# Performance work log

Measured on AMD Instinct MI355X. Metric: run time of the kernel, lower is better.

The kernel has to match this reference:

```python
import jax, jax.numpy as jnp
import numpy as np

B, BATCH, N, M, L1, NITER = 8, 4096, 16, 128, 16, 5


def setup_inputs() -> dict:
    key = jax.random.key(0)
    k1, k2, k3 = jax.random.split(key, 3)
    h = jax.random.normal(k1, (B, BATCH, N, M), dtype=jnp.float32)
    wd_init = jax.random.normal(k2, (B, BATCH, L1, N), dtype=jnp.float32)
    hyp = jax.random.uniform(k3, (NITER, B + 1), dtype=jnp.float32) * 0.01  # step sizes
    return {"h": h, "wd_init": wd_init, "hyp": hyp, "n": N, "l1": L1, "b": B, "num_of_iter": NITER}


def _herm(x):
    # inputs are real float32, so conj() in the original is the identity
    return jnp.swapaxes(x, -1, -2)


def reference(h, wd_init, hyp, n, l1, b, num_of_iter):
    batch, m = h.shape[1], h.shape[3]
    eye = jnp.eye(n, dtype=h.dtype)
    nb = jnp.asarray(n * b, h.dtype)

    def renorm_scale(prod):
        # prod: (b, batch, r, c); torch: sqrt(n*b / sum_b ||prod||_F^2) -> (batch,)
        fro2 = jnp.sum(prod * prod, axis=(-2, -1))  # (b, batch)
        return jnp.sqrt(nb / jnp.sum(fro2, axis=0))[:, None, None]  # (batch,1,1)

    def cov(h_, wa_, wd_):
        t = h_ @ wa_ @ wd_  # (..., n, n)
        return eye + t @ _herm(t)

    def grad_wa(wa_, wd_):
        inv_t = _herm(jnp.linalg.inv(cov(h, wa_, wd_)))  # (b,batch,n,n)
        f2 = jnp.sum(_herm(h) @ inv_t @ h @ wa_ @ wd_ @ _herm(wd_), axis=0) / b  # (batch,m,l1)
        return jnp.broadcast_to(f2[None], (b, batch, m, l1))

    def grad_wd_i(h_i, wa0, wd_i):
        inv_t = _herm(jnp.linalg.inv(cov(h_i, wa0, wd_i)))  # (batch,n,n)
        return _herm(wa0) @ _herm(h_i) @ inv_t @ h_i @ wa0 @ wd_i / b  # (batch,l1,n)

    # init: wa from svd of mean channel (numpy svd in original -> constant wrt grads)
    _, _, vh = jnp.linalg.svd(jnp.mean(h, axis=0), full_matrices=True)  # (batch,m,m)
    vh = jax.lax.stop_gradient(vh)
    wa = jnp.broadcast_to(vh[:, :, :l1][None], (b, batch, m, l1))
    wd = renorm_scale(wa @ wd_init) * wd_init  # (b,batch,l1,n)

    objs = []
    for x in range(num_of_iter):
        wa_t = wa + hyp[x, 0] * grad_wa(wa, wd)
        wa = renorm_scale(wa_t @ wd) * wa_t
        wd_t = wd
        for i in range(b):  # sequential inner projected-gradient updates (as in original)
            g = grad_wd_i(h[i], wa[0], wd[i])
            wd_t = wd_t.at[i].set(wd[i] + hyp[x, i + 1] * g)
            wd = renorm_scale(wa @ wd_t) * wd_t
        _, logdet = jnp.linalg.slogdet(cov(h, wa, wd))  # det > 0 (I + PSD)
        objs.append(jnp.sum(logdet, axis=0) / b)  # (batch,)
    obj = jnp.stack(objs, axis=0)  # (num_of_iter, batch)
    return obj.T, wa, wd
```

## Files before the change

### kernel.cpp

```cpp
#include <hip/hip_runtime.h>
#include <math.h>

#define NBATCH 4096


__device__ __forceinline__ float wave64_sum(float v){
  #pragma unroll
  for(int off=32; off; off>>=1) v += __shfl_xor(v, off, 64);
  return v;
}

__device__ __forceinline__ void slartgf(float f, float g, float* cs, float* sn, float* r){
  if (g == 0.0f){ *cs = 1.0f; *sn = 0.0f; *r = f; }
  else if (f == 0.0f){ *cs = 0.0f; *sn = copysignf(1.0f, g); *r = fabsf(g); }
  else {
    float d = sqrtf(f*f + g*g);
    *cs = fabsf(f)/d;
    float rr = copysignf(d, f);
    *r = rr;
    *sn = g/rr;
  }
}

__device__ __forceinline__ void slas2f(float f, float g, float hh, float* ssmin, float* ssmax){
  float fa=fabsf(f), ga=fabsf(g), ha=fabsf(hh);
  float fhmn=fminf(fa,ha), fhmx=fmaxf(fa,ha);
  if (fhmn == 0.0f){
    *ssmin = 0.0f;
    if (fhmx == 0.0f) *ssmax = ga;
    else { float mx=fmaxf(fhmx,ga), mn=fminf(fhmx,ga); float q=mn/mx; *ssmax = mx*sqrtf(1.0f+q*q); }
  } else {
    if (ga < fhmx){
      float as_=1.0f+fhmn/fhmx;
      float at_=(fhmx-fhmn)/fhmx;
      float au_=(ga/fhmx); au_=au_*au_;
      float c_=2.0f/(sqrtf(as_*as_+au_)+sqrtf(at_*at_+au_));
      *ssmin=fhmn*c_;
      *ssmax=fhmx/c_;
    } else {
      float au_=fhmx/ga;
      if (au_==0.0f){ *ssmin=(fhmn*fhmx)/ga; *ssmax=ga; }
      else {
        float as_=1.0f+fhmn/fhmx;
        float at_=(fhmx-fhmn)/fhmx;
        float t1=as_*au_, t2=at_*au_;
        float c_=1.0f/(sqrtf(1.0f+t1*t1)+sqrtf(1.0f+t2*t2));
        float sm=(fhmn*c_)*au_;
        *ssmin=sm+sm;
        *ssmax=ga/(c_+c_);
      }
    }
  }
}

__device__ __forceinline__ void slasv2f(float f, float g, float hh,
    float* ssmin, float* ssmax, float* snr, float* csr, float* snl, float* csl){
  const float EPS2 = 5.9604644775390625e-08f;
  float ft=f, fa=fabsf(f), ht=hh, ha=fabsf(hh);
  int pmax=1;
  bool swap_=(ha>fa);
  if (swap_){ pmax=3; float tmp=ft; ft=ht; ht=tmp; tmp=fa; fa=ha; ha=tmp; }
  float gt=g, ga=fabsf(g);
  float clt=0.f, crt=0.f, slt=0.f, srt=0.f;
  if (ga==0.0f){ *ssmin=ha; *ssmax=fa; clt=1.f; crt=1.f; slt=0.f; srt=0.f; }
  else {
    bool gasmal=true;
    if (ga>fa){
      pmax=2;
      if ((fa/ga) < EPS2){
        gasmal=false;
        *ssmax=ga;
        if (ha>1.0f) *ssmin=fa/(ga/ha); else *ssmin=(fa/ga)*ha;
        clt=1.f; slt=ht/gt; srt=1.f; crt=ft/gt;
      }
    }
    if (gasmal){
      float d_=fa-ha;
      float l_;
      if (d_==fa) l_=1.0f; else l_=d_/fa;
      float m_=gt/ft;
      float t_=2.0f-l_;
      float mm=m_*m_, tt=t_*t_;
      float s_=sqrtf(tt+mm);
      float r_;
      if (l_==0.0f) r_=fabsf(m_); else r_=sqrtf(l_*l_+mm);
      float a_=0.5f*(s_+r_);
      *ssmin=ha/a_;
      *ssmax=fa*a_;
      if (mm==0.0f){
        if (l_==0.0f) t_=copysignf(2.0f,ft)*copysignf(1.0f,gt);
        else t_=gt/copysignf(d_,ft)+m_/t_;
      } else {
        t_=(m_/(s_+t_)+m_/(r_+l_))*(1.0f+a_);
      }
      l_=sqrtf(t_*t_+4.0f);
      crt=2.0f/l_;
      srt=t_/l_;
      clt=(crt+srt*m_)/a_;
      slt=(ht/ft)*srt/a_;
    }
  }
  if (swap_){ *csl=srt; *snl=crt; *csr=slt; *snr=clt; }
  else { *csl=clt; *snl=slt; *csr=crt; *snr=srt; }
  float tsign=0.f;
  if (pmax==1) tsign=copysignf(1.f,*csr)*copysignf(1.f,*csl)*copysignf(1.f,f);
  if (pmax==2) tsign=copysignf(1.f,*snr)*copysignf(1.f,*csl)*copysignf(1.f,g);
  if (pmax==3) tsign=copysignf(1.f,*snr)*copysignf(1.f,*snl)*copysignf(1.f,hh);
  *ssmax=copysignf(*ssmax,tsign);
  *ssmin=copysignf(*ssmin,tsign*copysignf(1.f,f)*copysignf(1.f,hh));
}

__global__ __launch_bounds__(64) void init_kernel(
    const float* __restrict__ h,
    const float* __restrict__ wd_init,
    float* __restrict__ out_wa,
    float* __restrict__ out_wd)
{
  const int batch = blockIdx.x;
  const int lane  = threadIdx.x;
  if (batch >= NBATCH) return;

  __shared__ float A[16][128];
  __shared__ float Qc[128][16];
  __shared__ float Lm[16][16];
  __shared__ float VTs[16][16];
  __shared__ float Wtop[16][16];
  __shared__ float tauL[16], tq[16], tp[16];
  __shared__ float dB[16], eB[16];
  volatile __shared__ float dsh[17];
  volatile __shared__ float esh[17];

  for(int e0=lane; e0<2048; e0+=64){
    int nn=e0>>7, mmi=e0&127;
    float s=0.f;
    #pragma unroll
    for(int i=0;i<8;i++) s += h[((size_t)(i*NBATCH+batch))*2048 + nn*128 + mmi];
    A[nn][mmi]=s*0.125f;
  }
  __syncthreads();

  for(int i=0;i<16;i++){
    float part=0.f;
    for(int j=i+1+lane;j<128;j+=64){ float v=A[i][j]; part+=v*v; }
    float xn2=wave64_sum(part);
    float alpha=A[i][i];
    float tau,beta,scal;
    if (xn2==0.0f){ tau=0.f; beta=alpha; scal=0.f; }
    else {
      beta=-copysignf(sqrtf(alpha*alpha+xn2), alpha);
      tau=(beta-alpha)/beta;
      scal=1.0f/(alpha-beta);
    }
    if (tau!=0.0f){
      for(int j=i+1+lane;j<128;j+=64) A[i][j]*=scal;
    }
    if (lane==0){ A[i][i]=beta; tauL[i]=tau; }
    __syncthreads();
    if (tau!=0.0f){
      for(int r=i+1;r<16;r++){
        float p=0.f;
        for(int j=i+1+lane;j<128;j+=64) p += A[r][j]*A[i][j];
        float w=wave64_sum(p) + A[r][i];
        float tw=tau*w;
        for(int j=i+1+lane;j<128;j+=64) A[r][j]-=tw*A[i][j];
        if (lane==0) A[r][i]-=tw;
      }
    }
    __syncthreads();
  }

  for(int j=0;j<16;j++){
    float c0 = (lane==j)?1.0f:0.0f;
    float c1 = 0.0f;
    for(int i=0;i<16;i++){
      float tau=tauL[i];
      float p=0.f;
      if (lane>i) p += A[i][lane]*c0;
      else if (lane==i) p += c0;
      p += A[i][64+lane]*c1;
      float w=wave64_sum(p);
      if (tau!=0.0f){
        float tw=tau*w;
        if (lane==i) c0 -= tw;
        else if (lane>i) c0 -= tw*A[i][lane];
        c1 -= tw*A[i][64+lane];
      }
    }
    Qc[lane][j]=c0;
    Qc[64+lane][j]=c1;
  }
  __syncthreads();

  for(int e0=lane;e0<256;e0+=64){ int r=e0>>4,c=e0&15; Lm[r][c]=(c<=r)?A[r][c]:0.0f; }
  __syncthreads();

  for(int i=0;i<16;i++){
    float alpha=Lm[i][i];
    float xn2=0.f;
    for(int r=i+1;r<16;r++){ float v=Lm[r][i]; xn2+=v*v; }
    float tauqi,beta,scal;
    if (xn2==0.0f){ tauqi=0.f; beta=alpha; scal=0.f; }
    else { beta=-copysignf(sqrtf(alpha*alpha+xn2),alpha); tauqi=(beta-alpha)/beta; scal=1.0f/(alpha-beta); }
    __syncthreads();
    if (lane==0){
      tq[i]=tauqi; dB[i]=beta;
      if (tauqi!=0.0f) for(int r=i+1;r<16;r++) Lm[r][i]*=scal;
    }
    __syncthreads();
    if (tauqi!=0.0f && lane>i && lane<16){
      int c=lane;
      float w=Lm[i][c];
      for(int r=i+1;r<16;r++) w += Lm[r][i]*Lm[r][c];
      float tw=tauqi*w;
      Lm[i][c]-=tw;
      for(int r=i+1;r<16;r++) Lm[r][c]-=tw*Lm[r][i];
    }
    __syncthreads();
    if (i<15){
      float alph2=Lm[i][i+1];
      float yn2=0.f;
      for(int c=i+2;c<16;c++){ float v=Lm[i][c]; yn2+=v*v; }
      float taupi,beta2,scal2;
      if (yn2==0.0f){ taupi=0.f; beta2=alph2; scal2=0.f; }
      else { beta2=-copysignf(sqrtf(alph2*alph2+yn2),alph2); taupi=(beta2-alph2)/beta2; scal2=1.0f/(alph2-beta2); }
      __syncthreads();
      if (lane==0){
        tp[i]=taupi; eB[i]=beta2;
        if (taupi!=0.0f) for(int c=i+2;c<16;c++) Lm[i][c]*=scal2;
      }
      __syncthreads();
      if (taupi!=0.0f && lane>i && lane<16){
        int r=lane;
        float w=Lm[r][i+1];
        for(int c=i+2;c<16;c++) w += Lm[i][c]*Lm[r][c];
        float tw=taupi*w;
        Lm[r][i+1]-=tw;
        for(int c=i+2;c<16;c++) Lm[r][c]-=tw*Lm[i][c];
      }
      __syncthreads();
    } else {
      if (lane==0) tp[i]=0.0f;
      __syncthreads();
    }
  }

  if (lane==0){
    for(int k=1;k<=16;k++) dsh[k]=dB[k-1];
    for(int k=1;k<=15;k++) esh[k]=eB[k-1];
  }
  if (lane<16){
    for(int r=0;r<16;r++) VTs[r][lane]=(r==lane)?1.0f:0.0f;
  }
  __syncthreads();
  {
    const float EPSB = 5.9604644775390625e-08f;
    const float UNFL = 1.1754943508222875e-38f;
    const float tolb = 10.0f*EPSB;
    float sminoa;
    {
      sminoa=fabsf(dsh[1]);
      if (sminoa!=0.0f){
        float mu=sminoa;
        for(int k=2;k<=16;k++){
          mu=fabsf(dsh[k])*(mu/(mu+fabsf(esh[k-1])));
          sminoa=fminf(sminoa,mu);
          if (sminoa==0.0f) break;
        }
      }
      sminoa*=0.25f;
    }
    float thresh=fmaxf(tolb*sminoa, 6.0f*256.0f*UNFL);
    int maxitdivn=6*16, iterdivn=0, iter_=-1;
    int oldll=-1, oldm=-1, idir=0;
    int mq=16;
    float sminl=0.0f;
    int guard=0;
    while (guard++ < 4000){
      if (mq<=1) break;
      if (iter_>=16){ iter_-=16; iterdivn++; if (iterdivn>=maxitdivn) break; }
      float smax=fabsf(dsh[mq]);
      int ll=0; bool split=false;
      for(int lll=1;lll<=mq-1;lll++){
        int l2=mq-lll;
        float abss=fabsf(dsh[l2]);
        float abse=fabsf(esh[l2]);
        if (abse<=thresh){ ll=l2; split=true; break; }
        smax=fmaxf(smax,fmaxf(abss,abse));
      }
      if (split){
        if (lane==0) esh[ll]=0.0f;
        if (ll==mq-1){ mq=mq-1; continue; }
        ll=ll+1;
      } else ll=1;
      if (ll==mq-1){
        float sigmn,sigmx,sinr,cosr,sinl_,cosl_;
        slasv2f(dsh[mq-1],esh[mq-1],dsh[mq],&sigmn,&sigmx,&sinr,&cosr,&sinl_,&cosl_);
        if (lane==0){ dsh[mq-1]=sigmx; esh[mq-1]=0.0f; dsh[mq]=sigmn; }
        if (lane<16){
          float x0=VTs[mq-2][lane], y0=VTs[mq-1][lane];
          VTs[mq-2][lane]=cosr*x0+sinr*y0;
          VTs[mq-1][lane]=cosr*y0-sinr*x0;
        }
        mq-=2;
        continue;
      }
      if (ll>oldm || mq<oldll)
        idir=(fabsf(dsh[ll])>=fabsf(dsh[mq]))?1:2;
      bool conv=false;
      if (idir==1){
        if (fabsf(esh[mq-1])<=tolb*fabsf(dsh[mq])){ if(lane==0) esh[mq-1]=0.0f; conv=true; }
        if (!conv){
          float mu=fabsf(dsh[ll]); sminl=mu;
          for(int lll=ll;lll<=mq-1;lll++){
            if (fabsf(esh[lll])<=tolb*mu){ if(lane==0) esh[lll]=0.0f; conv=true; break; }
            mu=fabsf(dsh[lll+1])*(mu/(mu+fabsf(esh[lll])));
            sminl=fminf(sminl,mu);
          }
        }
      } else {
        if (fabsf(esh[ll])<=tolb*fabsf(dsh[ll])){ if(lane==0) esh[ll]=0.0f; conv=true; }
        if (!conv){
          float mu=fabsf(dsh[mq]); sminl=mu;
          for(int lll=mq-1;lll>=ll;lll--){
            if (fabsf(esh[lll])<=tolb*mu){ if(lane==0) esh[lll]=0.0f; conv=true; break; }
            mu=fabsf(dsh[lll])*(mu/(mu+fabsf(esh[lll])));
            sminl=fminf(sminl,mu);
          }
        }
      }
      if (conv) continue;
      oldll=ll; oldm=mq;
      float shift=0.0f, rdum;
      if (!( 16.0f*tolb*(sminl/smax) <= fmaxf(EPSB, 0.01f*tolb) )){
        float sll;
        if (idir==1){ sll=fabsf(dsh[ll]); slas2f(dsh[mq-1],esh[mq-1],dsh[mq],&shift,&rdum); }
        else        { sll=fabsf(dsh[mq]); slas2f(dsh[ll],esh[ll],dsh[ll+1],&shift,&rdum); }
        if (sll>0.0f){ float q=shift/sll; if (q*q<EPSB) shift=0.0f; }
      }
      iter_ += mq-ll;
      if (shift==0.0f){
        if (idir==1){
          float cs=1.0f, oldcs=1.0f, sn=0.0f, oldsn=0.0f, r1, r2;
          for(int i=ll;i<=mq-1;i++){
            slartgf(dsh[i]*cs, esh[i], &cs, &sn, &r1);
            if (i>ll){ if(lane==0) esh[i-1]=oldsn*r1; }
            slartgf(oldcs*r1, dsh[i+1]*sn, &oldcs, &oldsn, &r2);
            if (lane==0) dsh[i]=r2;
            if (lane<16){
              float lo=VTs[i-1][lane], hi=VTs[i][lane];
              VTs[i][lane]  =cs*hi-sn*lo;
              VTs[i-1][lane]=sn*hi+cs*lo;
            }
          }
          float hval=dsh[mq]*cs;
          float nd=hval*oldcs, ne=hval*oldsn;
          if (lane==0){ dsh[mq]=nd; esh[mq-1]=(fabsf(ne)<=thresh)?0.0f:ne; }
        } else {
          float cs=1.0f, oldcs=1.0f, sn=0.0f, oldsn=0.0f, r1, r2;
          for(int i=mq;i>=ll+1;i--){
            slartgf(dsh[i]*cs, esh[i-1], &cs, &sn, &r1);
            if (i<mq){ if(lane==0) esh[i]=oldsn*r1; }
            slartgf(oldcs*r1, dsh[i-1]*sn, &oldcs, &oldsn, &r2);
            if (lane==0) dsh[i]=r2;
            if (lane<16){
              float lo=VTs[i-2][lane], hi=VTs[i-1][lane];
              float c_=oldcs, s_=-oldsn;
              VTs[i-1][lane]=c_*hi-s_*lo;
              VTs[i-2][lane]=s_*hi+c_*lo;
            }
          }
          float hval=dsh[ll]*cs;
          float nd=hval*oldcs, ne=hval*oldsn;
          if (lane==0){ dsh[ll]=nd; esh[ll]=(fabsf(ne)<=thresh)?0.0f:ne; }
        }
      } else {
        if (idir==1){
          float dll=dsh[ll];
          float f=(fabsf(dll)-shift)*(copysignf(1.0f,dll)+shift/dll);
          float g=esh[ll];
          float cosr,sinr,cosl_,sinl_,r1;
          for(int i=ll;i<=mq-1;i++){
            slartgf(f,g,&cosr,&sinr,&r1);
            if (i>ll){ if(lane==0) esh[i-1]=r1; }
            float di=dsh[i], ei=esh[i], dip=dsh[i+1];
            f=cosr*di+sinr*ei;
            float ei1=cosr*ei-sinr*di;
            g=sinr*dip;
            float dip1=cosr*dip;
            slartgf(f,g,&cosl_,&sinl_,&r1);
            if (lane==0) dsh[i]=r1;
            f=cosl_*ei1+sinl_*dip1;
            float dip2=cosl_*dip1-sinl_*ei1;
            float eip2=0.0f;
            if (i<mq-1){
              float eip=esh[i+1];
              g=sinl_*eip;
              eip2=cosl_*eip;
            }
            if (lane==0){
              esh[i]=ei1;
              dsh[i+1]=dip2;
              if (i<mq-1) esh[i+1]=eip2;
            }
            if (lane<16){
              float lo=VTs[i-1][lane], hi=VTs[i][lane];
              VTs[i][lane]  =cosr*hi-sinr*lo;
              VTs[i-1][lane]=sinr*hi+cosr*lo;
            }
          }
          if (lane==0) esh[mq-1]=(fabsf(f)<=thresh)?0.0f:f;
        } else {
          float dm=dsh[mq];
          float f=(fabsf(dm)-shift)*(copysignf(1.0f,dm)+shift/dm);
          float g=esh[mq-1];
          float cosr,sinr,cosl_,sinl_,r1;
          for(int i=mq;i>=ll+1;i--){
            slartgf(f,g,&cosr,&sinr,&r1);
            if (i<mq){ if(lane==0) esh[i]=r1; }
            float di=dsh[i], eim=esh[i-1], dim=dsh[i-1];
            f=cosr*di+sinr*eim;
            float eim1=cosr*eim-sinr*di;
            g=sinr*dim;
            float dim1=cosr*dim;
            slartgf(f,g,&cosl_,&sinl_,&r1);
            if (lane==0) dsh[i]=r1;
            f=cosl_*eim1+sinl_*dim1;
            float dim2=cosl_*dim1-sinl_*eim1;
            float eim3=0.0f;
            if (i>ll+1){
              float e2=esh[i-2];
              g=sinl_*e2;
              eim3=cosl_*e2;
            }
            if (lane==0){
              esh[i-1]=eim1;
              dsh[i-1]=dim2;
              if (i>ll+1) esh[i-2]=eim3;
            }
            if (lane<16){
              float lo=VTs[i-2][lane], hi=VTs[i-1][lane];
              float c_=cosl_, s_=-sinl_;
              VTs[i-1][lane]=c_*hi-s_*lo;
              VTs[i-2][lane]=s_*hi+c_*lo;
            }
          }
          if (lane==0) esh[ll]=(fabsf(f)<=thresh)?0.0f:f;
        }
      }
    }
    for(int k=1;k<=16;k++){
      float dv=dsh[k];
      if (dv<0.0f){
        if (lane==0) dsh[k]=-dv;
        if (lane<16) VTs[k-1][lane]=-VTs[k-1][lane];
      }
    }
    for(int i=1;i<=15;i++){
      int isub=1; float smn=dsh[1];
      for(int j=2;j<=17-i;j++){ float dj=dsh[j]; if (dj<=smn){ isub=j; smn=dj; } }
      if (isub!=17-i){
        if (lane==0){ dsh[isub]=dsh[17-i]; dsh[17-i]=smn; }
        if (lane<16){ float tv=VTs[isub-1][lane]; VTs[isub-1][lane]=VTs[16-i][lane]; VTs[16-i][lane]=tv; }
      }
    }
  }
  __syncthreads();

  for(int i=14;i>=0;i--){
    float tau=tp[i];
    if (tau!=0.0f && lane<16){
      int r=lane;
      float w=VTs[r][i+1];
      for(int c=i+2;c<16;c++) w += VTs[r][c]*Lm[i][c];
      float tw=tau*w;
      VTs[r][i+1]-=tw;
      for(int c=i+2;c<16;c++) VTs[r][c]-=tw*Lm[i][c];
    }
  }
  __syncthreads();

  for(int e0=lane;e0<256;e0+=64){
    int r=e0>>4, j=e0&15;
    float s=0.f;
    #pragma unroll
    for(int c=0;c<16;c++) s += VTs[r][c]*Qc[c][j];
    Wtop[r][j]=s;
  }
  __syncthreads();
  for(int e0=lane;e0<2048;e0+=64){
    int r=e0>>4, j=e0&15;
    out_wa[(size_t)batch*2048 + e0] = (r<16)?Wtop[r][j]:Qc[r][j];
  }

  float part=0.f;
  for(int i=0;i<8;i++){
    const float* wdi = wd_init + ((size_t)(i*NBATCH+batch))*256;
    for(int e=lane;e<256;e+=64) ((float*)Lm)[e]=wdi[e];
    __syncthreads();
    for(int e0=lane;e0<2048;e0+=64){
      int r=e0>>4, j=e0&15;
      float s=0.f;
      #pragma unroll
      for(int c=0;c<16;c++){
        float wav=(r<16)?Wtop[r][c]:Qc[r][c];
        s += wav*((float*)Lm)[c*16+j];
      }
      part += s*s;
    }
    __syncthreads();
  }
  float fro2=wave64_sum(part);
  float scal2=sqrtf(128.0f/fro2);
  for(int i=0;i<8;i++){
    const float* wdi = wd_init + ((size_t)(i*NBATCH+batch))*256;
    float* wdo = out_wd + ((size_t)(i*NBATCH+batch))*256;
    for(int e=lane;e<256;e+=64) wdo[e]=scal2*wdi[e];
  }
}

__global__ __launch_bounds__(256) void iter_kernel(
    const float* __restrict__ h,
    const float* __restrict__ hyp,
    float* __restrict__ out_obj,
    float* __restrict__ out_wa,
    float* __restrict__ out_wd)
{
  const int batch = blockIdx.x;
  const int t = threadIdx.x;
  if (batch >= NBATCH) return;

  __shared__ float Wf[2048];
  __shared__ __align__(16) float Hs[2048];
  __shared__ float Uf[2048];
  __shared__ float Wdf[2048];
  __shared__ float Wdtf[2048];
  __shared__ float Cvf[2048];
  __shared__ float F2f[2048];
  __shared__ float Gmf[256];
  __shared__ float T1f[256];
  __shared__ float T2f[256];
  __shared__ float T3f[256];
  __shared__ float redbuf[4];
  __shared__ float bcv[2];
  __shared__ float hyps[45];
  __shared__ float logdets[8];

  const int r16 = t>>4, c16 = t&15;

  {
    const float* src = out_wa + (size_t)batch*2048;
    for(int e=t;e<2048;e+=256) Wf[e]=src[e];
    for(int i=0;i<8;i++){
      const float* s2 = out_wd + ((size_t)(i*NBATCH+batch))*256;
      Wdf[i*256+t]=s2[t];
    }
    if (t<45) hyps[t]=hyp[t];
  }
  __syncthreads();

  auto stage_h = [&](int i){
    const float4* h4 = reinterpret_cast<const float4*>(h + ((size_t)(i*NBATCH+batch))*2048);
    float4* s4 = reinterpret_cast<float4*>(Hs);
    s4[t]=h4[t];
    s4[t+256]=h4[t+256];
  };
  auto compute_u = [&](int i){
    const float4* Hs4 = reinterpret_cast<const float4*>(Hs);
    float s=0.f;
    #pragma unroll
    for(int m4=0;m4<32;m4++){
      float4 hv=Hs4[r16*32+m4];
      s += hv.x*Wf[(m4*4+0)*16+c16];
      s += hv.y*Wf[(m4*4+1)*16+c16];
      s += hv.z*Wf[(m4*4+2)*16+c16];
      s += hv.w*Wf[(m4*4+3)*16+c16];
    }
    Uf[i*256+t]=s;
  };
  auto block_red = [&](float v)->float{
    #pragma unroll
    for(int off=32;off;off>>=1) v += __shfl_xor(v, off, 64);
    if ((t&63)==0) redbuf[t>>6]=v;
    __syncthreads();
    if (t==0) bcv[0]=redbuf[0]+redbuf[1]+redbuf[2]+redbuf[3];
    __syncthreads();
    return bcv[0];
  };
  auto batched_gj = [&](){
    int ii=t>>5, ss=t&31;
    float logacc=0.f;
    for(int k=0;k<16;k++){
      float piv=Cvf[ii*256+k*16+k];
      float rk8[8],ck8[8],cur8[8];
      #pragma unroll
      for(int q=0;q<8;q++){
        int e=ss*8+q; int rr=e>>4, cc=e&15;
        rk8[q]=Cvf[ii*256+k*16+cc];
        ck8[q]=Cvf[ii*256+rr*16+k];
        cur8[q]=Cvf[ii*256+e];
      }
      __syncthreads();
      float pinv=1.0f/piv;
      if (ss==0) logacc += logf(piv);
      #pragma unroll
      for(int q=0;q<8;q++){
        int e=ss*8+q; int rr=e>>4, cc=e&15;
        float v;
        if (rr==k) v=(cc==k)?pinv:rk8[q]*pinv;
        else if (cc==k) v=-ck8[q]*pinv;
        else v=cur8[q]-ck8[q]*pinv*rk8[q];
        Cvf[ii*256+e]=v;
      }
      __syncthreads();
    }
    if (ss==0) logdets[ii]=logacc;
    __syncthreads();
  };
  auto build_cov_all = [&](){
    for(int i=0;i<8;i++){
      float s=0.f;
      #pragma unroll
      for(int k=0;k<16;k++) s += Uf[i*256+r16*16+k]*Wdf[i*256+k*16+c16];
      T1f[t]=s;
      __syncthreads();
      float cv=(r16==c16)?1.0f:0.0f;
      #pragma unroll
      for(int k=0;k<16;k++) cv += T1f[r16*16+k]*T1f[c16*16+k];
      Cvf[i*256+t]=cv;
      __syncthreads();
    }
  };

  for(int i=0;i<8;i++){ stage_h(i); __syncthreads(); compute_u(i); __syncthreads(); }

  for(int x=0;x<5;x++){
    build_cov_all();
    batched_gj();
    if (x>0 && t==0){
      float s=0.f;
      for(int i=0;i<8;i++) s+=logdets[i];
      out_obj[batch*5+(x-1)]=s*0.125f;
    }
    for(int e=t;e<2048;e+=256) F2f[e]=0.f;
    __syncthreads();
    for(int i=0;i<8;i++){
      float s=0.f;
      #pragma unroll
      for(int k=0;k<16;k++) s += Cvf[i*256+k*16+r16]*Uf[i*256+k*16+c16];
      T1f[t]=s; __syncthreads();
      s=0.f;
      #pragma unroll
      for(int k=0;k<16;k++) s += T1f[r16*16+k]*Wdf[i*256+k*16+c16];
      T2f[t]=s; __syncthreads();
      s=0.f;
      #pragma unroll
      for(int k=0;k<16;k++) s += T2f[r16*16+k]*Wdf[i*256+c16*16+k];
      T3f[t]=s; __syncthreads();
      stage_h(i); __syncthreads();
      {
        int mm=t>>1, l0=(t&1)*8;
        float a0=0,a1=0,a2=0,a3=0,a4=0,a5=0,a6=0,a7=0;
        #pragma unroll
        for(int nn=0;nn<16;nn++){
          float hv=Hs[nn*128+mm];
          const float* T3r=&T3f[nn*16+l0];
          a0+=hv*T3r[0]; a1+=hv*T3r[1]; a2+=hv*T3r[2]; a3+=hv*T3r[3];
          a4+=hv*T3r[4]; a5+=hv*T3r[5]; a6+=hv*T3r[6]; a7+=hv*T3r[7];
        }
        float* F2r=&F2f[mm*16+l0];
        F2r[0]+=a0; F2r[1]+=a1; F2r[2]+=a2; F2r[3]+=a3;
        F2r[4]+=a4; F2r[5]+=a5; F2r[6]+=a6; F2r[7]+=a7;
      }
      __syncthreads();
    }
    {
      float hyp0=hyps[x*9]*0.125f;
      for(int e=t;e<2048;e+=256) Wf[e] += hyp0*F2f[e];
      __syncthreads();
      float s=0.f;
      #pragma unroll 8
      for(int mmi=0;mmi<128;mmi++) s += Wf[mmi*16+r16]*Wf[mmi*16+c16];
      Gmf[t]=s;
      __syncthreads();
      float part=0.f;
      for(int j=0;j<8;j++){
        float gw=0.f;
        #pragma unroll
        for(int k=0;k<16;k++) gw += Gmf[r16*16+k]*Wdf[j*256+k*16+c16];
        part += gw*Wdf[j*256+t];
      }
      float fro2=block_red(part);
      float scal=sqrtf(128.0f/fro2);
      for(int e=t;e<2048;e+=256) Wf[e]*=scal;
      Gmf[t]*=scal*scal;
      __syncthreads();
    }
    for(int i=0;i<8;i++){ stage_h(i); __syncthreads(); compute_u(i); __syncthreads(); }
    for(int e=t;e<2048;e+=256) Wdtf[e]=Wdf[e];
    __syncthreads();
    for(int i=0;i<8;i++){
      float s=0.f;
      #pragma unroll
      for(int k=0;k<16;k++) s += Uf[i*256+r16*16+k]*Wdf[i*256+k*16+c16];
      T1f[t]=s; __syncthreads();
      float cv=(r16==c16)?1.0f:0.0f;
      #pragma unroll
      for(int k=0;k<16;k++) cv += T1f[r16*16+k]*T1f[c16*16+k];
      T2f[t]=cv; __syncthreads();
      for(int k=0;k<16;k++){
        float piv=T2f[k*16+k];
        float rk=T2f[k*16+c16];
        float ck=T2f[r16*16+k];
        float cur=T2f[t];
        __syncthreads();
        float pinv=1.0f/piv;
        float v;
        if (r16==k) v=(c16==k)?pinv:rk*pinv;
        else if (c16==k) v=-ck*pinv;
        else v=cur-ck*pinv*rk;
        T2f[t]=v;
        __syncthreads();
      }
      s=0.f;
      #pragma unroll
      for(int k=0;k<16;k++) s += Uf[i*256+k*16+r16]*T2f[c16*16+k];
      T1f[t]=s; __syncthreads();
      s=0.f;
      #pragma unroll
      for(int k=0;k<16;k++) s += T1f[r16*16+k]*Uf[i*256+k*16+c16];
      T3f[t]=s; __syncthreads();
      {
        float g=0.f;
        #pragma unroll
        for(int k=0;k<16;k++) g += T3f[r16*16+k]*Wdf[i*256+k*16+c16];
        g*=0.125f;
        Wdtf[i*256+t]=Wdf[i*256+t]+hyps[x*9+i+1]*g;
      }
      __syncthreads();
      {
        float part=0.f;
        for(int j=0;j<8;j++){
          float gw=0.f;
          #pragma unroll
          for(int k=0;k<16;k++) gw += Gmf[r16*16+k]*Wdtf[j*256+k*16+c16];
          part += gw*Wdtf[j*256+t];
        }
        float fro2=block_red(part);
        float scal=sqrtf(128.0f/fro2);
        for(int e=t;e<2048;e+=256) Wdf[e]=scal*Wdtf[e];
      }
      __syncthreads();
    }
  }
  build_cov_all();
  batched_gj();
  if (t==0){
    float s=0.f;
    for(int i=0;i<8;i++) s+=logdets[i];
    out_obj[batch*5+4]=s*0.125f;
  }
  __syncthreads();
  for(int i=0;i<8;i++){
    float* dst = out_wa + ((size_t)(i*NBATCH+batch))*2048;
    for(int e=t;e<2048;e+=256) dst[e]=Wf[e];
  }
  for(int i=0;i<8;i++){
    float* dst = out_wd + ((size_t)(i*NBATCH+batch))*256;
    dst[t]=Wdf[i*256+t];
  }
}

extern "C" void kernel_launch(void* const* d_in, const int* in_sizes, int n_in,
                              void* d_out, int out_size, void* d_ws, size_t ws_size,
                              hipStream_t stream)
{
  (void)in_sizes; (void)n_in; (void)d_ws; (void)ws_size; (void)out_size;
  const float* h   = (const float*)d_in[0];
  const float* wdi = (const float*)d_in[1];
  const float* hyp = (const float*)d_in[2];
  float* out = (float*)d_out;
  float* out_obj = out;
  float* out_wa  = out + (size_t)NBATCH*5;
  float* out_wd  = out_wa + (size_t)8*NBATCH*128*16;

  init_kernel<<<NBATCH, 64, 0, stream>>>(h, wdi, out_wa, out_wd);
  iter_kernel<<<NBATCH, 256, 0, stream>>>(h, hyp, out_obj, out_wa, out_wd);
}
```

Baseline: 6.291 ms.

## Restructure iteration kernel into per-wave 16x16 chains with swizzled shared memory

Rewrites the iteration kernel so each wave processes its own channels' 16x16 covariance, Gauss-Jordan inversion and gradient chain, using compiler barriers in place of block-wide syncs. Shared memory shrinks: fewer buffers, half-size H staging, and an XOR-style rotate swizzle to avoid bank conflicts. The renormalisation is folded lazily into the next step, and launch bounds request higher occupancy. The init kernel keeps Q columns in registers and adds syncs in the SVD loop. The main risks are wave-level races that rely on implicit lockstep, and serialisation of the inner updates onto one wave.

```diff
diff --git a/kernel.cpp b/kernel.cpp
--- a/kernel.cpp
+++ b/kernel.cpp
@@ -3,12 +3,16 @@
 
 #define NBATCH 4096
 
+#define WBAR() asm volatile("" ::: "memory")
+
+__device__ __forceinline__ int SW(int r, int c){ return (r<<4) | (((c)+(r))&15); }
 
 __device__ __forceinline__ float wave64_sum(float v){
   #pragma unroll
   for(int off=32; off; off>>=1) v += __shfl_xor(v, off, 64);
   return v;
 }
+
 
 __device__ __forceinline__ void slartgf(float f, float g, float* cs, float* sn, float* r){
   if (g == 0.0f){ *cs = 1.0f; *sn = 0.0f; *r = f; }
@@ -118,17 +122,16 @@
 {
   const int batch = blockIdx.x;
   const int lane  = threadIdx.x;
-  if (batch >= NBATCH) return;
 
   __shared__ float A[16][128];
-  __shared__ float Qc[128][16];
   __shared__ float Lm[16][16];
   __shared__ float VTs[16][16];
   __shared__ float Wtop[16][16];
-  __shared__ float tauL[16], tq[16], tp[16];
+  __shared__ float Qtop[256];
+  __shared__ float tauL[16], tp[16];
   __shared__ float dB[16], eB[16];
-  volatile __shared__ float dsh[17];
-  volatile __shared__ float esh[17];
+  __shared__ float dsh[17];
+  __shared__ float esh[17];
 
   for(int e0=lane; e0<2048; e0+=64){
     int nn=e0>>7, mmi=e0&127;
@@ -169,6 +172,8 @@
     __syncthreads();
   }
 
+  float qc0[16], qc1[16];
+  #pragma unroll
   for(int j=0;j<16;j++){
     float c0 = (lane==j)?1.0f:0.0f;
     float c1 = 0.0f;
@@ -186,8 +191,12 @@
         c1 -= tw*A[i][64+lane];
       }
     }
-    Qc[lane][j]=c0;
-    Qc[64+lane][j]=c1;
+    qc0[j]=c0;
+    qc1[j]=c1;
+  }
+  if (lane<16){
+    #pragma unroll
+    for(int j=0;j<16;j++) Qtop[lane*16+j]=qc0[j];
   }
   __syncthreads();
 
@@ -203,7 +212,7 @@
     else { beta=-copysignf(sqrtf(alpha*alpha+xn2),alpha); tauqi=(beta-alpha)/beta; scal=1.0f/(alpha-beta); }
     __syncthreads();
     if (lane==0){
-      tq[i]=tauqi; dB[i]=beta;
+      dB[i]=beta;
       if (tauqi!=0.0f) for(int r=i+1;r<16;r++) Lm[r][i]*=scal;
     }
     __syncthreads();
@@ -289,18 +298,21 @@
       }
       if (split){
         if (lane==0) esh[ll]=0.0f;
+        __syncthreads();
         if (ll==mq-1){ mq=mq-1; continue; }
         ll=ll+1;
       } else ll=1;
       if (ll==mq-1){
         float sigmn,sigmx,sinr,cosr,sinl_,cosl_;
         slasv2f(dsh[mq-1],esh[mq-1],dsh[mq],&sigmn,&sigmx,&sinr,&cosr,&sinl_,&cosl_);
+        __syncthreads();
         if (lane==0){ dsh[mq-1]=sigmx; esh[mq-1]=0.0f; dsh[mq]=sigmn; }
         if (lane<16){
           float x0=VTs[mq-2][lane], y0=VTs[mq-1][lane];
           VTs[mq-2][lane]=cosr*x0+sinr*y0;
           VTs[mq-1][lane]=cosr*y0-sinr*x0;
         }
+        __syncthreads();
         mq-=2;
         continue;
       }
@@ -328,7 +340,7 @@
           }
         }
       }
-      if (conv) continue;
+      if (conv){ __syncthreads(); continue; }
       oldll=ll; oldm=mq;
       float shift=0.0f, rdum;
       if (!( 16.0f*tolb*(sminl/smax) <= fmaxf(EPSB, 0.01f*tolb) )){
@@ -351,10 +363,12 @@
               VTs[i][lane]  =cs*hi-sn*lo;
               VTs[i-1][lane]=sn*hi+cs*lo;
             }
+            __syncthreads();
           }
           float hval=dsh[mq]*cs;
           float nd=hval*oldcs, ne=hval*oldsn;
           if (lane==0){ dsh[mq]=nd; esh[mq-1]=(fabsf(ne)<=thresh)?0.0f:ne; }
+          __syncthreads();
         } else {
           float cs=1.0f, oldcs=1.0f, sn=0.0f, oldsn=0.0f, r1, r2;
           for(int i=mq;i>=ll+1;i--){
@@ -368,10 +382,12 @@
               VTs[i-1][lane]=c_*hi-s_*lo;
               VTs[i-2][lane]=s_*hi+c_*lo;
             }
+            __syncthreads();
           }
           float hval=dsh[ll]*cs;
           float nd=hval*oldcs, ne=hval*oldsn;
           if (lane==0){ dsh[ll]=nd; esh[ll]=(fabsf(ne)<=thresh)?0.0f:ne; }
+          __syncthreads();
         }
       } else {
         if (idir==1){
@@ -407,8 +423,10 @@
               VTs[i][lane]  =cosr*hi-sinr*lo;
               VTs[i-1][lane]=sinr*hi+cosr*lo;
             }
+            __syncthreads();
           }
           if (lane==0) esh[mq-1]=(fabsf(f)<=thresh)?0.0f:f;
+          __syncthreads();
         } else {
           float dm=dsh[mq];
           float f=(fabsf(dm)-shift)*(copysignf(1.0f,dm)+shift/dm);
@@ -443,8 +461,10 @@
               VTs[i-1][lane]=c_*hi-s_*lo;
               VTs[i-2][lane]=s_*hi+c_*lo;
             }
+            __syncthreads();
           }
           if (lane==0) esh[ll]=(fabsf(f)<=thresh)?0.0f:f;
+          __syncthreads();
         }
       }
     }
@@ -454,6 +474,7 @@
         if (lane==0) dsh[k]=-dv;
         if (lane<16) VTs[k-1][lane]=-VTs[k-1][lane];
       }
+      __syncthreads();
     }
     for(int i=1;i<=15;i++){
       int isub=1; float smn=dsh[1];
@@ -462,6 +483,7 @@
         if (lane==0){ dsh[isub]=dsh[17-i]; dsh[17-i]=smn; }
         if (lane<16){ float tv=VTs[isub-1][lane]; VTs[isub-1][lane]=VTs[16-i][lane]; VTs[16-i][lane]=tv; }
       }
+      __syncthreads();
     }
   }
   __syncthreads();
@@ -476,38 +498,44 @@
       VTs[r][i+1]-=tw;
       for(int c=i+2;c<16;c++) VTs[r][c]-=tw*Lm[i][c];
     }
-  }
-  __syncthreads();
+    __syncthreads();
+  }
 
   for(int e0=lane;e0<256;e0+=64){
     int r=e0>>4, j=e0&15;
     float s=0.f;
     #pragma unroll
-    for(int c=0;c<16;c++) s += VTs[r][c]*Qc[c][j];
+    for(int c=0;c<16;c++) s += VTs[r][c]*Qtop[c*16+j];
     Wtop[r][j]=s;
   }
   __syncthreads();
-  for(int e0=lane;e0<2048;e0+=64){
-    int r=e0>>4, j=e0&15;
-    out_wa[(size_t)batch*2048 + e0] = (r<16)?Wtop[r][j]:Qc[r][j];
-  }
-
+
+  {
+    float* wab = out_wa + (size_t)batch*2048;
+    #pragma unroll
+    for(int j=0;j<16;j++){
+      wab[lane*16+j]      = (lane<16)? Wtop[lane][j] : qc0[j];
+      wab[(lane+64)*16+j] = qc1[j];
+    }
+  }
+
+  float wrow[16];
+  #pragma unroll
+  for(int c=0;c<16;c++) wrow[c] = (lane<16)? Wtop[lane][c] : qc0[c];
+  float* wdL = (float*)Lm;
   float part=0.f;
   for(int i=0;i<8;i++){
     const float* wdi = wd_init + ((size_t)(i*NBATCH+batch))*256;
-    for(int e=lane;e<256;e+=64) ((float*)Lm)[e]=wdi[e];
-    __syncthreads();
-    for(int e0=lane;e0<2048;e0+=64){
-      int r=e0>>4, j=e0&15;
-      float s=0.f;
-      #pragma unroll
-      for(int c=0;c<16;c++){
-        float wav=(r<16)?Wtop[r][c]:Qc[r][c];
-        s += wav*((float*)Lm)[c*16+j];
-      }
-      part += s*s;
-    }
-    __syncthreads();
+    __syncthreads();
+    for(int e=lane;e<256;e+=64) wdL[e]=wdi[e];
+    __syncthreads();
+    #pragma unroll
+    for(int j=0;j<16;j++){
+      float s0=0.f, s1=0.f;
+      #pragma unroll
+      for(int c=0;c<16;c++){ float wv=wdL[c*16+j]; s0 += wrow[c]*wv; s1 += qc1[c]*wv; }
+      part += s0*s0 + s1*s1;
+    }
   }
   float fro2=wave64_sum(part);
   float scal2=sqrtf(128.0f/fro2);
@@ -518,7 +546,7 @@
   }
 }
 
-__global__ __launch_bounds__(256) void iter_kernel(
+__global__ __launch_bounds__(256,4) void iter_kernel(
     const float* __restrict__ h,
     const float* __restrict__ hyp,
     float* __restrict__ out_obj,
@@ -527,246 +555,341 @@
 {
   const int batch = blockIdx.x;
   const int t = threadIdx.x;
-  if (batch >= NBATCH) return;
+  const int wave = t>>6, lane = t&63;
+  const int r16 = t>>4, c16 = t&15;
+  const int ls = lane>>4, cc = lane&15;
 
   __shared__ float Wf[2048];
-  __shared__ __align__(16) float Hs[2048];
   __shared__ float Uf[2048];
-  __shared__ float Wdf[2048];
-  __shared__ float Wdtf[2048];
-  __shared__ float Cvf[2048];
-  __shared__ float F2f[2048];
-  __shared__ float Gmf[256];
-  __shared__ float T1f[256];
-  __shared__ float T2f[256];
-  __shared__ float T3f[256];
-  __shared__ float redbuf[4];
-  __shared__ float bcv[2];
-  __shared__ float hyps[45];
-  __shared__ float logdets[8];
-
-  const int r16 = t>>4, c16 = t&15;
+  __shared__ float Kf[2048];
+  __shared__ float Wd[2048];
+  __shared__ __align__(16) float Hs[1024];
+  __shared__ float Gm[256];
+  __shared__ float misc[24];
+
+  auto chain_K = [&](int ch, bool wlog){
+    float* U = Uf + ch*256;
+    float* W = Wd + ch*256;
+    float* A = Kf + ch*256;
+    float* B = Hs + wave*256;
+    #pragma unroll
+    for(int q=0;q<4;q++){
+      int rr=q*4+ls; float s=0.f;
+      #pragma unroll
+      for(int k=0;k<16;k++) s += U[rr*16+k]*W[SW(k,cc)];
+      A[SW(rr,cc)]=s;
+    }
+    WBAR();
+    #pragma unroll
+    for(int q=0;q<4;q++){
+      int rr=q*4+ls; float s=(rr==cc)?1.0f:0.0f;
+      #pragma unroll
+      for(int k=0;k<16;k++) s += A[SW(rr,k)]*A[SW(cc,k)];
+      B[SW(rr,cc)]=s;
+    }
+    WBAR();
+    float logacc=0.f;
+    for(int k=0;k<16;k++){
+      float piv=B[SW(k,k)];
+      float pinv=1.0f/piv;
+      if (wlog) logacc += logf(piv);
+      float rkv=B[SW(k,cc)];
+      float ck[4],cu[4];
+      #pragma unroll
+      for(int q=0;q<4;q++){ int rr=q*4+ls; ck[q]=B[SW(rr,k)]; cu[q]=B[SW(rr,cc)]; }
+      WBAR();
+      #pragma unroll
+      for(int q=0;q<4;q++){
+        int rr=q*4+ls; float v;
+        if (rr==k) v=(cc==k)?pinv:rkv*pinv;
+        else if (cc==k) v=-ck[q]*pinv;
+        else v=cu[q]-ck[q]*pinv*rkv;
+        B[SW(rr,cc)]=v;
+      }
+      WBAR();
+    }
+    if (wlog && lane==0) misc[ch]=logacc;
+    #pragma unroll
+    for(int q=0;q<4;q++){
+      int rr=q*4+ls; float s=0.f;
+      #pragma unroll
+      for(int k=0;k<16;k++) s += B[SW(k,rr)]*U[k*16+cc];
+      A[SW(rr,cc)]=s;
+    }
+    WBAR();
+    #pragma unroll
+    for(int q=0;q<4;q++){
+      int rr=q*4+ls; float s=0.f;
+      #pragma unroll
+      for(int k=0;k<16;k++) s += A[SW(rr,k)]*W[SW(k,cc)];
+      B[SW(rr,cc)]=s;
+    }
+    WBAR();
+    #pragma unroll
+    for(int q=0;q<4;q++){
+      int rr=q*4+ls; float s=0.f;
+      #pragma unroll
+      for(int k=0;k<16;k++) s += B[SW(rr,k)]*W[SW(cc,k)];
+      A[SW(rr,cc)]=s;
+    }
+    WBAR();
+  };
+
+  auto inner_step = [&](int i, int x, bool first){
+    float sc;
+    if (first) sc = 1.0f;
+    else {
+      float fs=0.f;
+      #pragma unroll
+      for(int j=0;j<8;j++) fs += misc[8+j];
+      sc = sqrtf(128.0f/fs);
+    }
+    float* U = Uf + i*256;
+    float* W = Wd + i*256;
+    float* A = Hs;
+    float* B = Hs + 256;
+    #pragma unroll
+    for(int q=0;q<4;q++){
+      int rr=q*4+ls; float s=0.f;
+      #pragma unroll
+      for(int k=0;k<16;k++) s += U[rr*16+k]*(sc*W[SW(k,cc)]);
+      A[SW(rr,cc)]=s;
+    }
+    WBAR();
+    #pragma unroll
+    for(int q=0;q<4;q++){
+      int rr=q*4+ls; float s=(rr==cc)?1.0f:0.0f;
+      #pragma unroll
+      for(int k=0;k<16;k++) s += A[SW(rr,k)]*A[SW(cc,k)];
+      B[SW(rr,cc)]=s;
+    }
+    WBAR();
+    for(int k=0;k<16;k++){
+      float piv=B[SW(k,k)];
+      float pinv=1.0f/piv;
+      float rkv=B[SW(k,cc)];
+      float ck[4],cu[4];
+      #pragma unroll
+      for(int q=0;q<4;q++){ int rr=q*4+ls; ck[q]=B[SW(rr,k)]; cu[q]=B[SW(rr,cc)]; }
+      WBAR();
+      #pragma unroll
+      for(int q=0;q<4;q++){
+        int rr=q*4+ls; float v;
+        if (rr==k) v=(cc==k)?pinv:rkv*pinv;
+        else if (cc==k) v=-ck[q]*pinv;
+        else v=cu[q]-ck[q]*pinv*rkv;
+        B[SW(rr,cc)]=v;
+      }
+      WBAR();
+    }
+    #pragma unroll
+    for(int q=0;q<4;q++){
+      int rr=q*4+ls; float s=0.f;
+      #pragma unroll
+      for(int k=0;k<16;k++) s += U[k*16+rr]*B[SW(cc,k)];
+      A[SW(rr,cc)]=s;
+    }
+    WBAR();
+    #pragma unroll
+    for(int q=0;q<4;q++){
+      int rr=q*4+ls; float s=0.f;
+      #pragma unroll
+      for(int k=0;k<16;k++) s += A[SW(rr,k)]*U[k*16+cc];
+      B[SW(rr,cc)]=s;
+    }
+    WBAR();
+    float hypi = hyp[x*9+i+1];
+    float wnew[4];
+    #pragma unroll
+    for(int q=0;q<4;q++){
+      int rr=q*4+ls; float g=0.f;
+      #pragma unroll
+      for(int k=0;k<16;k++) g += B[SW(rr,k)]*(sc*W[SW(k,cc)]);
+      g*=0.125f;
+      wnew[q] = sc*W[SW(rr,cc)] + hypi*g;
+    }
+    WBAR();
+    #pragma unroll
+    for(int q=0;q<4;q++){ int rr=q*4+ls; W[SW(rr,cc)]=wnew[q]; }
+    WBAR();
+    float part=0.f;
+    #pragma unroll
+    for(int q=0;q<4;q++){
+      int rr=q*4+ls; float gw=0.f;
+      #pragma unroll
+      for(int k=0;k<16;k++) gw += Gm[rr*16+k]*W[SW(k,cc)];
+      part += gw*W[SW(rr,cc)];
+    }
+    part = wave64_sum(part);
+    if (lane==0) misc[8+i]=part;
+  };
+
+  auto stage_and_u = [&](int ch, int half){
+    const float4* h4 = (const float4*)(h + ((size_t)(ch*NBATCH+batch))*2048);
+    __syncthreads();
+    ((float4*)Hs)[t] = h4[half*256+t];
+    __syncthreads();
+    if ((r16>>3)==half){
+      const float4* H4=(const float4*)Hs;
+      float s=0.f;
+      #pragma unroll
+      for(int m4=0;m4<32;m4++){
+        float4 hv=H4[(r16&7)*32+m4];
+        s += hv.x*Wf[(m4*4+0)*16+c16];
+        s += hv.y*Wf[(m4*4+1)*16+c16];
+        s += hv.z*Wf[(m4*4+2)*16+c16];
+        s += hv.w*Wf[(m4*4+3)*16+c16];
+      }
+      Uf[ch*256+r16*16+c16]=s;
+    }
+  };
 
   {
     const float* src = out_wa + (size_t)batch*2048;
     for(int e=t;e<2048;e+=256) Wf[e]=src[e];
-    for(int i=0;i<8;i++){
-      const float* s2 = out_wd + ((size_t)(i*NBATCH+batch))*256;
-      Wdf[i*256+t]=s2[t];
-    }
-    if (t<45) hyps[t]=hyp[t];
+    for(int ch=0;ch<8;ch++){
+      const float* s2 = out_wd + ((size_t)(ch*NBATCH+batch))*256;
+      Wd[ch*256+SW(r16,c16)] = s2[t];
+    }
+    if (t<8) misc[8+t]=16.0f;
   }
   __syncthreads();
-
-  auto stage_h = [&](int i){
-    const float4* h4 = reinterpret_cast<const float4*>(h + ((size_t)(i*NBATCH+batch))*2048);
-    float4* s4 = reinterpret_cast<float4*>(Hs);
-    s4[t]=h4[t];
-    s4[t+256]=h4[t+256];
-  };
-  auto compute_u = [&](int i){
-    const float4* Hs4 = reinterpret_cast<const float4*>(Hs);
-    float s=0.f;
-    #pragma unroll
-    for(int m4=0;m4<32;m4++){
-      float4 hv=Hs4[r16*32+m4];
-      s += hv.x*Wf[(m4*4+0)*16+c16];
-      s += hv.y*Wf[(m4*4+1)*16+c16];
-      s += hv.z*Wf[(m4*4+2)*16+c16];
-      s += hv.w*Wf[(m4*4+3)*16+c16];
-    }
-    Uf[i*256+t]=s;
-  };
-  auto block_red = [&](float v)->float{
-    #pragma unroll
-    for(int off=32;off;off>>=1) v += __shfl_xor(v, off, 64);
-    if ((t&63)==0) redbuf[t>>6]=v;
-    __syncthreads();
-    if (t==0) bcv[0]=redbuf[0]+redbuf[1]+redbuf[2]+redbuf[3];
-    __syncthreads();
-    return bcv[0];
-  };
-  auto batched_gj = [&](){
-    int ii=t>>5, ss=t&31;
-    float logacc=0.f;
-    for(int k=0;k<16;k++){
-      float piv=Cvf[ii*256+k*16+k];
-      float rk8[8],ck8[8],cur8[8];
-      #pragma unroll
-      for(int q=0;q<8;q++){
-        int e=ss*8+q; int rr=e>>4, cc=e&15;
-        rk8[q]=Cvf[ii*256+k*16+cc];
-        ck8[q]=Cvf[ii*256+rr*16+k];
-        cur8[q]=Cvf[ii*256+e];
-      }
-      __syncthreads();
-      float pinv=1.0f/piv;
-      if (ss==0) logacc += logf(piv);
-      #pragma unroll
-      for(int q=0;q<8;q++){
-        int e=ss*8+q; int rr=e>>4, cc=e&15;
-        float v;
-        if (rr==k) v=(cc==k)?pinv:rk8[q]*pinv;
-        else if (cc==k) v=-ck8[q]*pinv;
-        else v=cur8[q]-ck8[q]*pinv*rk8[q];
-        Cvf[ii*256+e]=v;
-      }
-      __syncthreads();
-    }
-    if (ss==0) logdets[ii]=logacc;
-    __syncthreads();
-  };
-  auto build_cov_all = [&](){
-    for(int i=0;i<8;i++){
-      float s=0.f;
-      #pragma unroll
-      for(int k=0;k<16;k++) s += Uf[i*256+r16*16+k]*Wdf[i*256+k*16+c16];
-      T1f[t]=s;
-      __syncthreads();
-      float cv=(r16==c16)?1.0f:0.0f;
-      #pragma unroll
-      for(int k=0;k<16;k++) cv += T1f[r16*16+k]*T1f[c16*16+k];
-      Cvf[i*256+t]=cv;
-      __syncthreads();
-    }
-  };
-
-  for(int i=0;i<8;i++){ stage_h(i); __syncthreads(); compute_u(i); __syncthreads(); }
+  for(int ch=0;ch<8;ch++)
+    for(int half=0;half<2;half++)
+      stage_and_u(ch,half);
+  __syncthreads();
 
   for(int x=0;x<5;x++){
-    build_cov_all();
-    batched_gj();
+    {
+      float fs=0.f;
+      #pragma unroll
+      for(int j=0;j<8;j++) fs += misc[8+j];
+      float scf = sqrtf(128.0f/fs);
+      #pragma unroll
+      for(int ci=0;ci<2;ci++){
+        float* W = Wd + (wave+ci*4)*256;
+        #pragma unroll
+        for(int q=0;q<4;q++){ int rr=q*4+ls; W[SW(rr,cc)]*=scf; }
+      }
+      WBAR();
+    }
+    chain_K(wave, true);
+    chain_K(wave+4, true);
+    __syncthreads();
     if (x>0 && t==0){
       float s=0.f;
-      for(int i=0;i<8;i++) s+=logdets[i];
-      out_obj[batch*5+(x-1)]=s*0.125f;
-    }
-    for(int e=t;e<2048;e+=256) F2f[e]=0.f;
-    __syncthreads();
-    for(int i=0;i<8;i++){
-      float s=0.f;
-      #pragma unroll
-      for(int k=0;k<16;k++) s += Cvf[i*256+k*16+r16]*Uf[i*256+k*16+c16];
-      T1f[t]=s; __syncthreads();
-      s=0.f;
-      #pragma unroll
-      for(int k=0;k<16;k++) s += T1f[r16*16+k]*Wdf[i*256+k*16+c16];
-      T2f[t]=s; __syncthreads();
-      s=0.f;
-      #pragma unroll
-      for(int k=0;k<16;k++) s += T2f[r16*16+k]*Wdf[i*256+c16*16+k];
-      T3f[t]=s; __syncthreads();
-      stage_h(i); __syncthreads();
-      {
-        int mm=t>>1, l0=(t&1)*8;
-        float a0=0,a1=0,a2=0,a3=0,a4=0,a5=0,a6=0,a7=0;
-        #pragma unroll
-        for(int nn=0;nn<16;nn++){
-          float hv=Hs[nn*128+mm];
-          const float* T3r=&T3f[nn*16+l0];
-          a0+=hv*T3r[0]; a1+=hv*T3r[1]; a2+=hv*T3r[2]; a3+=hv*T3r[3];
-          a4+=hv*T3r[4]; a5+=hv*T3r[5]; a6+=hv*T3r[6]; a7+=hv*T3r[7];
+      #pragma unroll
+      for(int j=0;j<8;j++) s+=misc[j];
+      out_obj[(size_t)batch*5+(x-1)]=s*0.125f;
+    }
+    float a0=0,a1=0,a2=0,a3=0,a4=0,a5=0,a6=0,a7=0;
+    {
+      int mm=t>>1, l0=(t&1)*8;
+      for(int ch=0;ch<8;ch++){
+        const float4* h4 = (const float4*)(h + ((size_t)(ch*NBATCH+batch))*2048);
+        const float* Kr = Kf + ch*256;
+        for(int half=0;half<2;half++){
+          __syncthreads();
+          ((float4*)Hs)[t] = h4[half*256+t];
+          __syncthreads();
+          #pragma unroll
+          for(int n=0;n<8;n++){
+            float hv=Hs[n*128+mm];
+            int n8=half*8+n;
+            a0 += hv*Kr[SW(n8,l0+0)];
+            a1 += hv*Kr[SW(n8,l0+1)];
+            a2 += hv*Kr[SW(n8,l0+2)];
+            a3 += hv*Kr[SW(n8,l0+3)];
+            a4 += hv*Kr[SW(n8,l0+4)];
+            a5 += hv*Kr[SW(n8,l0+5)];
+            a6 += hv*Kr[SW(n8,l0+6)];
+            a7 += hv*Kr[SW(n8,l0+7)];
+          }
         }
-        float* F2r=&F2f[mm*16+l0];
-        F2r[0]+=a0; F2r[1]+=a1; F2r[2]+=a2; F2r[3]+=a3;
-        F2r[4]+=a4; F2r[5]+=a5; F2r[6]+=a6; F2r[7]+=a7;
-      }
-      __syncthreads();
+      }
     }
     {
-      float hyp0=hyps[x*9]*0.125f;
-      for(int e=t;e<2048;e+=256) Wf[e] += hyp0*F2f[e];
+      float hyp0 = hyp[x*9]*0.125f;
+      int mm=t>>1, l0=(t&1)*8;
+      float* F2r=&Wf[mm*16+l0];
+      F2r[0]+=hyp0*a0; F2r[1]+=hyp0*a1; F2r[2]+=hyp0*a2; F2r[3]+=hyp0*a3;
+      F2r[4]+=hyp0*a4; F2r[5]+=hyp0*a5; F2r[6]+=hyp0*a6; F2r[7]+=hyp0*a7;
       __syncthreads();
       float s=0.f;
       #pragma unroll 8
-      for(int mmi=0;mmi<128;mmi++) s += Wf[mmi*16+r16]*Wf[mmi*16+c16];
-      Gmf[t]=s;
+      for(int m=0;m<128;m++) s += Wf[m*16+r16]*Wf[m*16+c16];
+      Gm[t]=s;
       __syncthreads();
       float part=0.f;
       for(int j=0;j<8;j++){
         float gw=0.f;
         #pragma unroll
-        for(int k=0;k<16;k++) gw += Gmf[r16*16+k]*Wdf[j*256+k*16+c16];
-        part += gw*Wdf[j*256+t];
-      }
-      float fro2=block_red(part);
-      float scal=sqrtf(128.0f/fro2);
+        for(int k=0;k<16;k++) gw += Gm[r16*16+k]*Wd[j*256+SW(k,c16)];
+        part += gw*Wd[j*256+SW(r16,c16)];
+      }
+      part = wave64_sum(part);
+      if (lane==0) misc[16+wave]=part;
+      __syncthreads();
+      float fro2 = misc[16]+misc[17]+misc[18]+misc[19];
+      float scal = sqrtf(128.0f/fro2);
       for(int e=t;e<2048;e+=256) Wf[e]*=scal;
-      Gmf[t]*=scal*scal;
+      Gm[t]*=scal*scal;
+    }
+    __syncthreads();
+    for(int ch=0;ch<8;ch++)
+      for(int half=0;half<2;half++)
+        stage_and_u(ch,half);
+    __syncthreads();
+    #pragma unroll
+    for(int ci=0;ci<2;ci++){
+      int ch=wave+ci*4;
+      float* W = Wd + ch*256;
+      float part=0.f;
+      #pragma unroll
+      for(int q=0;q<4;q++){
+        int rr=q*4+ls; float gw=0.f;
+        #pragma unroll
+        for(int k=0;k<16;k++) gw += Gm[rr*16+k]*W[SW(k,cc)];
+        part += gw*W[SW(rr,cc)];
+      }
+      part=wave64_sum(part);
+      if (lane==0) misc[8+ch]=part;
+    }
+    __syncthreads();
+    for(int i=0;i<8;i++){
+      if (wave==(i&3)) inner_step(i,x,(i==0));
       __syncthreads();
     }
-    for(int i=0;i<8;i++){ stage_h(i); __syncthreads(); compute_u(i); __syncthreads(); }
-    for(int e=t;e<2048;e+=256) Wdtf[e]=Wdf[e];
-    __syncthreads();
-    for(int i=0;i<8;i++){
-      float s=0.f;
-      #pragma unroll
-      for(int k=0;k<16;k++) s += Uf[i*256+r16*16+k]*Wdf[i*256+k*16+c16];
-      T1f[t]=s; __syncthreads();
-      float cv=(r16==c16)?1.0f:0.0f;
-      #pragma unroll
-      for(int k=0;k<16;k++) cv += T1f[r16*16+k]*T1f[c16*16+k];
-      T2f[t]=cv; __syncthreads();
-      for(int k=0;k<16;k++){
-        float piv=T2f[k*16+k];
-        float rk=T2f[k*16+c16];
-        float ck=T2f[r16*16+k];
-        float cur=T2f[t];
-        __syncthreads();
-        float pinv=1.0f/piv;
-        float v;
-        if (r16==k) v=(c16==k)?pinv:rk*pinv;
-        else if (c16==k) v=-ck*pinv;
-        else v=cur-ck*pinv*rk;
-        T2f[t]=v;
-        __syncthreads();
-      }
-      s=0.f;
-      #pragma unroll
-      for(int k=0;k<16;k++) s += Uf[i*256+k*16+r16]*T2f[c16*16+k];
-      T1f[t]=s; __syncthreads();
-      s=0.f;
-      #pragma unroll
-      for(int k=0;k<16;k++) s += T1f[r16*16+k]*Uf[i*256+k*16+c16];
-      T3f[t]=s; __syncthreads();
-      {
-        float g=0.f;
-        #pragma unroll
-        for(int k=0;k<16;k++) g += T3f[r16*16+k]*Wdf[i*256+k*16+c16];
-        g*=0.125f;
-        Wdtf[i*256+t]=Wdf[i*256+t]+hyps[x*9+i+1]*g;
-      }
-      __syncthreads();
-      {
-        float part=0.f;
-        for(int j=0;j<8;j++){
-          float gw=0.f;
-          #pragma unroll
-          for(int k=0;k<16;k++) gw += Gmf[r16*16+k]*Wdtf[j*256+k*16+c16];
-          part += gw*Wdtf[j*256+t];
-        }
-        float fro2=block_red(part);
-        float scal=sqrtf(128.0f/fro2);
-        for(int e=t;e<2048;e+=256) Wdf[e]=scal*Wdtf[e];
-      }
-      __syncthreads();
-    }
-  }
-  build_cov_all();
-  batched_gj();
+  }
+
+  {
+    float fs=0.f;
+    #pragma unroll
+    for(int j=0;j<8;j++) fs += misc[8+j];
+    float scf = sqrtf(128.0f/fs);
+    #pragma unroll
+    for(int ci=0;ci<2;ci++){
+      float* W = Wd + (wave+ci*4)*256;
+      #pragma unroll
+      for(int q=0;q<4;q++){ int rr=q*4+ls; W[SW(rr,cc)]*=scf; }
+    }
+    WBAR();
+  }
+  chain_K(wave, true);
+  chain_K(wave+4, true);
+  __syncthreads();
   if (t==0){
     float s=0.f;
-    for(int i=0;i<8;i++) s+=logdets[i];
-    out_obj[batch*5+4]=s*0.125f;
-  }
-  __syncthreads();
-  for(int i=0;i<8;i++){
-    float* dst = out_wa + ((size_t)(i*NBATCH+batch))*2048;
+    #pragma unroll
+    for(int j=0;j<8;j++) s+=misc[j];
+    out_obj[(size_t)batch*5+4]=s*0.125f;
+  }
+  for(int ch=0;ch<8;ch++){
+    float* dst = out_wa + ((size_t)(ch*NBATCH+batch))*2048;
     for(int e=t;e<2048;e+=256) dst[e]=Wf[e];
   }
-  for(int i=0;i<8;i++){
-    float* dst = out_wd + ((size_t)(i*NBATCH+batch))*256;
-    dst[t]=Wdf[i*256+t];
+  for(int ch=0;ch<8;ch++){
+    out_wd[((size_t)(ch*NBATCH+batch))*256 + t] = Wd[ch*256+SW(r16,c16)];
   }
 }
 
```

After: 9.849 ms. 56.6% more time.
